# Optimization experiments

Measured on AMD Instinct MI355X. Metric: run time of the kernel, lower is better.

The kernel has to match this reference:

```python
import math
import jax, jax.numpy as jnp
import numpy as np

L, H, C, T_MAX, V = 4, 12, 768, 1024, 50257
D = C // H
EPS = 1e-5


def setup_inputs() -> dict:
    key = jax.random.key(0)
    ks = iter(jax.random.split(key, 32))
    s = 0.02
    inp = {
        "idx": jax.random.randint(next(ks), (2, 1024), 0, V, dtype=jnp.int32),
        "wte": jax.random.normal(next(ks), (V, C), jnp.float32) * s,
        "wpe": jax.random.normal(next(ks), (T_MAX, C), jnp.float32) * s,
        # per-layer stacked params, weights stored [in, out]
        "ln1_w": jnp.ones((L, C), jnp.float32),
        "ln1_b": jnp.zeros((L, C), jnp.float32),
        "qkv_w": jax.random.normal(next(ks), (L, C, 3 * C), jnp.float32) * s,
        "qkv_b": jnp.zeros((L, 3 * C), jnp.float32),
        "proj_w": jax.random.normal(next(ks), (L, C, C), jnp.float32) * (s / math.sqrt(2 * L)),
        "proj_b": jnp.zeros((L, C), jnp.float32),
        "ln2_w": jnp.ones((L, C), jnp.float32),
        "ln2_b": jnp.zeros((L, C), jnp.float32),
        "fc_w": jax.random.normal(next(ks), (L, C, 4 * C), jnp.float32) * s,
        "fc_b": jnp.zeros((L, 4 * C), jnp.float32),
        "fc2_w": jax.random.normal(next(ks), (L, 4 * C, C), jnp.float32) * (s / math.sqrt(2 * L)),
        "fc2_b": jnp.zeros((L, C), jnp.float32),
        "lnf_w": jnp.ones((C,), jnp.float32),
        "lnf_b": jnp.zeros((C,), jnp.float32),
        "head_w": jax.random.normal(next(ks), (C, V), jnp.float32) * s,
    }
    return inp


def _layernorm(x, w, b):
    mu = jnp.mean(x, axis=-1, keepdims=True)
    var = jnp.mean(jnp.square(x - mu), axis=-1, keepdims=True)
    return (x - mu) * jax.lax.rsqrt(var + EPS) * w + b


def _new_gelu(x):
    k = math.sqrt(2.0 / math.pi)
    return 0.5 * x * (1.0 + jnp.tanh(k * (x + 0.044715 * x * x * x)))


def _gpt_forward(idx, wte, wpe, layer_params, lnf_w, lnf_b, head_w):
    B, T = idx.shape
    x = wte[idx] + wpe[:T][None, :, :]  # [B, T, C]
    causal = jnp.tril(jnp.ones((T, T), bool))

    def block(x, p):
        ln1w, ln1b, qkvw, qkvb, pw, pb, ln2w, ln2b, fcw, fcb, fc2w, fc2b = p
        h = _layernorm(x, ln1w, ln1b)
        qkv = h @ qkvw + qkvb  # [B, T, 3C]
        q, k, v = jnp.split(qkv, 3, axis=-1)
        # [B, H, T, D]
        q = q.reshape(B, T, H, D).transpose(0, 2, 1, 3)
        k = k.reshape(B, T, H, D).transpose(0, 2, 1, 3)
        v = v.reshape(B, T, H, D).transpose(0, 2, 1, 3)
        att = jnp.einsum("bhtd,bhsd->bhts", q, k) * (1.0 / math.sqrt(D))
        att = jnp.where(causal, att, -jnp.inf)
        att = jax.nn.softmax(att, axis=-1)
        y = jnp.einsum("bhts,bhsd->bhtd", att, v)
        y = y.transpose(0, 2, 1, 3).reshape(B, T, C)
        x = x + (y @ pw + pb)
        h2 = _layernorm(x, ln2w, ln2b)
        m = _new_gelu(h2 @ fcw + fcb) @ fc2w + fc2b
        return x + m, None

    x, _ = jax.lax.scan(block, x, layer_params)
    x = _layernorm(x, lnf_w, lnf_b)
    logits = x @ head_w  # [B, T, V]
    return logits.reshape(B * T, V)


def reference(idx, wte, wpe, ln1_w, ln1_b, qkv_w, qkv_b, proj_w, proj_b,
              ln2_w, ln2_b, fc_w, fc_b, fc2_w, fc2_b, lnf_w, lnf_b, head_w):
    layer_params = (ln1_w, ln1_b, qkv_w, qkv_b, proj_w, proj_b,
                    ln2_w, ln2_b, fc_w, fc_b, fc2_w, fc2_b)
    return _gpt_forward(idx, wte, wpe, layer_params, lnf_w, lnf_b, head_w)
```

## Files before the change

kernel.cpp:

```cpp
#include <hip/hip_runtime.h>
#include <hip/hip_bf16.h>

typedef __hip_bfloat16 bf16;
typedef __attribute__((ext_vector_type(8))) short bf16x8;
typedef __attribute__((ext_vector_type(4))) float f32x4;
typedef __attribute__((ext_vector_type(4), aligned(4))) float f32x4u;

#define NL 4
#define NH 12
#define C 768
#define T 1024
#define NB 2
#define BTOK 2048
#define V 50257
#define DH 64

__device__ __forceinline__ void gload16(const void* g, void* l) {
  __builtin_amdgcn_global_load_lds(
      (const __attribute__((address_space(1))) void*)g,
      (__attribute__((address_space(3))) void*)l, 16, 0, 0);
}

__device__ __forceinline__ float block_sum(float v, float* red) {
#pragma unroll
  for (int off = 32; off; off >>= 1) v += __shfl_down(v, off);
  int lane = threadIdx.x & 63, wid = threadIdx.x >> 6;
  __syncthreads();
  if (lane == 0) red[wid] = v;
  __syncthreads();
  return red[0] + red[1] + red[2] + red[3];
}

__global__ __launch_bounds__(256) void k_embed(const int* __restrict__ idx,
    const float* __restrict__ wte, const float* __restrict__ wpe,
    float* __restrict__ x) {
  long i = (long)blockIdx.x * 256 + threadIdx.x;
  int bt = (int)(i / C), c = (int)(i % C);
  int t = bt & (T - 1);
  x[i] = wte[(long)idx[bt] * C + c] + wpe[(long)t * C + c];
}

__global__ __launch_bounds__(256) void k_transpose_bf16(const float* __restrict__ W,
    bf16* __restrict__ Wt, int K, int N) {
  __shared__ float tile[32][33];
  long zoff = (long)blockIdx.z * K * N;
  W += zoff;
  Wt += zoff;
  int n0 = blockIdx.x * 32, k0 = blockIdx.y * 32;
  int tx = threadIdx.x, ty = threadIdx.y;
#pragma unroll
  for (int i = 0; i < 4; i++) {
    int k = k0 + ty + i * 8, n = n0 + tx;
    if (k < K && n < N) tile[ty + i * 8][tx] = W[(long)k * N + n];
  }
  __syncthreads();
#pragma unroll
  for (int i = 0; i < 4; i++) {
    int n = n0 + ty + i * 8, k = k0 + tx;
    if (n < N && k < K) Wt[(long)n * K + k] = __float2bfloat16(tile[tx][ty + i * 8]);
  }
}

__global__ __launch_bounds__(256) void k_layernorm(const float* __restrict__ x,
    const float* __restrict__ w, const float* __restrict__ b, bf16* __restrict__ out) {
  __shared__ float red[4];
  long row = blockIdx.x;
  const float* xr = x + row * C;
  int t = threadIdx.x;
  float v0 = xr[t], v1 = xr[t + 256], v2 = xr[t + 512];
  float s = block_sum(v0 + v1 + v2, red);
  float mu = s * (1.0f / C);
  float d0 = v0 - mu, d1 = v1 - mu, d2 = v2 - mu;
  float vs = block_sum(d0 * d0 + d1 * d1 + d2 * d2, red);
  float inv = rsqrtf(vs * (1.0f / C) + 1e-5f);
  bf16* orow = out + row * C;
  orow[t]       = __float2bfloat16(d0 * inv * w[t]       + b[t]);
  orow[t + 256] = __float2bfloat16(d1 * inv * w[t + 256] + b[t + 256]);
  orow[t + 512] = __float2bfloat16(d2 * inv * w[t + 512] + b[t + 512]);
}

__global__ __launch_bounds__(256) void k_attn(const bf16* __restrict__ q,
    const bf16* __restrict__ k, const bf16* __restrict__ vt,
    bf16* __restrict__ yb) {
  __shared__ __align__(16) bf16 Pl[4][16][72];
  int pr = blockIdx.x, bh = blockIdx.y;
  int b = bh / NH, h = bh % NH;
  int tid = threadIdx.x, w = tid >> 6, lane = tid & 63;
  int l15 = lane & 15, hi = lane >> 4;
  const bf16* qbase = q + (long)bh * T * DH;
  const bf16* kbase = k + (long)bh * T * DH;
  const bf16* vbase = vt + (long)bh * DH * T;

  for (int s2 = 0; s2 < 2; s2++) {
    int qt = s2 ? (T / 64 - 1 - pr) : pr;
    int qrow = qt * 64 + w * 16 + l15;
    bf16x8 qf0 = *(const bf16x8*)(qbase + (long)qrow * DH + hi * 8);
    bf16x8 qf1 = *(const bf16x8*)(qbase + (long)qrow * DH + 32 + hi * 8);

    f32x4 accy[4] = {};
    float m_run = -1e30f, l_run = 0.f;

    int nkt = qt + 1;
    for (int kt = 0; kt < nkt; kt++) {
      int kv0 = kt * 64;
      f32x4 accs[4] = {};
#pragma unroll
      for (int kvi = 0; kvi < 4; kvi++) {
        const bf16* kr = kbase + (long)(kv0 + kvi * 16 + l15) * DH + hi * 8;
        bf16x8 kf0 = *(const bf16x8*)kr;
        bf16x8 kf1 = *(const bf16x8*)(kr + 32);
        accs[kvi] = __builtin_amdgcn_mfma_f32_16x16x32_bf16(kf0, qf0, accs[kvi], 0, 0, 0);
        accs[kvi] = __builtin_amdgcn_mfma_f32_16x16x32_bf16(kf1, qf1, accs[kvi], 0, 0, 0);
      }
      bool diag = (kt == qt);
      float p[4][4];
      float tmax = -1e30f;
#pragma unroll
      for (int kvi = 0; kvi < 4; kvi++)
#pragma unroll
        for (int rr = 0; rr < 4; rr++) {
          float s = accs[kvi][rr];
          if (diag && (kvi * 16 + hi * 4 + rr > w * 16 + l15)) s = -1e30f;
          p[kvi][rr] = s;
          tmax = fmaxf(tmax, s);
        }
      tmax = fmaxf(tmax, __shfl_xor(tmax, 16));
      tmax = fmaxf(tmax, __shfl_xor(tmax, 32));
      float m_new = fmaxf(m_run, tmax);
      float scl = __expf(m_run - m_new);
      float psum = 0.f;
#pragma unroll
      for (int kvi = 0; kvi < 4; kvi++)
#pragma unroll
        for (int rr = 0; rr < 4; rr++) {
          float e = __expf(p[kvi][rr] - m_new);
          p[kvi][rr] = e;
          psum += e;
        }
      psum += __shfl_xor(psum, 16);
      psum += __shfl_xor(psum, 32);
      l_run = l_run * scl + psum;
      m_run = m_new;
#pragma unroll
      for (int rr = 0; rr < 4; rr++) {
        float sy = __shfl(scl, hi * 4 + rr);
#pragma unroll
        for (int j = 0; j < 4; j++) accy[j][rr] *= sy;
      }
#pragma unroll
      for (int kvi = 0; kvi < 4; kvi++) {
        union { bf16 hh[2]; unsigned u; } pk0, pk1;
        pk0.hh[0] = __float2bfloat16(p[kvi][0]);
        pk0.hh[1] = __float2bfloat16(p[kvi][1]);
        pk1.hh[0] = __float2bfloat16(p[kvi][2]);
        pk1.hh[1] = __float2bfloat16(p[kvi][3]);
        *(unsigned*)&Pl[w][l15][kvi * 16 + hi * 4]     = pk0.u;
        *(unsigned*)&Pl[w][l15][kvi * 16 + hi * 4 + 2] = pk1.u;
      }
#pragma unroll
      for (int c = 0; c < 2; c++) {
        bf16x8 pf = *(const bf16x8*)&Pl[w][l15][c * 32 + hi * 8];
#pragma unroll
        for (int j = 0; j < 4; j++) {
          const bf16* vr = vbase + (long)(j * 16 + l15) * T + kv0 + c * 32 + hi * 8;
          bf16x8 vf = *(const bf16x8*)vr;
          accy[j] = __builtin_amdgcn_mfma_f32_16x16x32_bf16(pf, vf, accy[j], 0, 0, 0);
        }
      }
    }
    float inv = 1.0f / l_run;
#pragma unroll
    for (int rr = 0; rr < 4; rr++) {
      float li = __shfl(inv, hi * 4 + rr);
      int qg = qt * 64 + w * 16 + hi * 4 + rr;
#pragma unroll
      for (int j = 0; j < 4; j++)
        yb[((long)(b * T + qg)) * C + h * DH + j * 16 + l15] =
            __float2bfloat16(accy[j][rr] * li);
    }
  }
}

__global__ __launch_bounds__(512, 1) void k_head(const bf16* __restrict__ A,
    const bf16* __restrict__ B, float* __restrict__ Cv) {
  __shared__ __align__(16) char lds[131072];
  int hw = blockIdx.y * 8 + blockIdx.x;
  int L = (hw & 7) * 197 + (hw >> 3);
  int mt = L & 7, nt = L >> 3;
  int m0 = mt * 256, n0 = nt * 256;
  int tid = threadIdx.x, lane = tid & 63, wid = tid >> 6;
  int wm = wid >> 2, wn = wid & 3;
  int l15 = lane & 15, hi = lane >> 4, l7 = lane & 7;
  int sg = (lane & 7) ^ (lane >> 3);
  int srA = wid * 8 + (lane >> 3);
  const bf16* Ab = A + (long)(m0 + srA) * 768 + sg * 8;
  const bf16* Bb = B + (long)(n0 + srA) * 768 + sg * 8;
  auto STAGE = [&](int tile, int h) {
    char* dst = lds + (tile & 1) * 65536 + h * 16384 + wid * 1024;
    const bf16* src = (h < 2 ? Ab : Bb) + (long)((h & 1) * 128) * 768 + tile * 64;
    gload16(src, dst);
    gload16(src + 64 * 768, dst + 8192);
  };
  f32x4 acc[8][4] = {};
  STAGE(0, 0); STAGE(0, 1); STAGE(0, 2); STAGE(0, 3); STAGE(1, 0);
  asm volatile("s_waitcnt vmcnt(2)" ::: "memory");
  __builtin_amdgcn_s_barrier();
  int bro = (wn & 1) * 64;
  int g0 = (hi ^ l7) * 16, g1 = ((4 + hi) ^ l7) * 16;
  for (int t = 0; t < 12; t++) {
    char* ha = lds + (t & 1) * 65536 + wm * 16384;
    char* hb = lds + (t & 1) * 65536 + 32768 + (wn >> 1) * 16384;
    bf16x8 af[4], bv[4];
#pragma unroll
    for (int mf = 0; mf < 4; mf++)
      af[mf] = *(const bf16x8*)(ha + (mf * 16 + l15) * 128 + g0);
#pragma unroll
    for (int nf = 0; nf < 4; nf++)
      bv[nf] = *(const bf16x8*)(hb + (bro + nf * 16 + l15) * 128 + g0);
    if (t + 1 < 12) { STAGE(t + 1, 1); STAGE(t + 1, 2); }
    __builtin_amdgcn_s_barrier();
    __builtin_amdgcn_s_setprio(1);
#pragma unroll
    for (int mf = 0; mf < 4; mf++)
#pragma unroll
      for (int nf = 0; nf < 4; nf++)
        acc[mf][nf] = __builtin_amdgcn_mfma_f32_16x16x32_bf16(af[mf], bv[nf], acc[mf][nf], 0, 0, 0);
    __builtin_amdgcn_s_setprio(0);
    __builtin_amdgcn_s_barrier();
#pragma unroll
    for (int mf = 0; mf < 4; mf++)
      af[mf] = *(const bf16x8*)(ha + ((mf + 4) * 16 + l15) * 128 + g0);
    if (t + 1 < 12) STAGE(t + 1, 3);
    __builtin_amdgcn_s_barrier();
    __builtin_amdgcn_s_setprio(1);
#pragma unroll
    for (int mf = 0; mf < 4; mf++)
#pragma unroll
      for (int nf = 0; nf < 4; nf++)
        acc[mf + 4][nf] = __builtin_amdgcn_mfma_f32_16x16x32_bf16(af[mf], bv[nf], acc[mf + 4][nf], 0, 0, 0);
    __builtin_amdgcn_s_setprio(0);
    __builtin_amdgcn_s_barrier();
#pragma unroll
    for (int mf = 0; mf < 4; mf++)
      af[mf] = *(const bf16x8*)(ha + (mf * 16 + l15) * 128 + g1);
#pragma unroll
    for (int nf = 0; nf < 4; nf++)
      bv[nf] = *(const bf16x8*)(hb + (bro + nf * 16 + l15) * 128 + g1);
    __builtin_amdgcn_s_barrier();
    __builtin_amdgcn_s_setprio(1);
#pragma unroll
    for (int mf = 0; mf < 4; mf++)
#pragma unroll
      for (int nf = 0; nf < 4; nf++)
        acc[mf][nf] = __builtin_amdgcn_mfma_f32_16x16x32_bf16(af[mf], bv[nf], acc[mf][nf], 0, 0, 0);
    __builtin_amdgcn_s_setprio(0);
    __builtin_amdgcn_s_barrier();
#pragma unroll
    for (int mf = 0; mf < 4; mf++)
      af[mf] = *(const bf16x8*)(ha + ((mf + 4) * 16 + l15) * 128 + g1);
    if (t + 2 < 12) STAGE(t + 2, 0);
    __builtin_amdgcn_s_barrier();
    __builtin_amdgcn_s_setprio(1);
#pragma unroll
    for (int mf = 0; mf < 4; mf++)
#pragma unroll
      for (int nf = 0; nf < 4; nf++)
        acc[mf + 4][nf] = __builtin_amdgcn_mfma_f32_16x16x32_bf16(af[mf], bv[nf], acc[mf + 4][nf], 0, 0, 0);
    __builtin_amdgcn_s_setprio(0);
    if (t < 11) {
      if (t + 2 < 12) asm volatile("s_waitcnt vmcnt(2)" ::: "memory");
      else            asm volatile("s_waitcnt vmcnt(0)" ::: "memory");
      __builtin_amdgcn_s_barrier();
    }
  }
  __syncthreads();
  float* Cst = (float*)lds;
#pragma unroll
  for (int mf = 0; mf < 8; mf++) {
#pragma unroll
    for (int nf = 0; nf < 4; nf++)
#pragma unroll
      for (int rr = 0; rr < 4; rr++)
        Cst[(wm * 16 + hi * 4 + rr) * 260 + wn * 64 + nf * 16 + l15] = acc[mf][nf][rr];
    __syncthreads();
#pragma unroll
    for (int s = 0; s < 4; s++) {
      int gid = tid + s * 512;
      int r = gid >> 6, g = gid & 63;
      int grow = m0 + (r >> 4) * 128 + mf * 16 + (r & 15);
      int gcol = n0 + g * 4;
      f32x4 vv = *(const f32x4*)&Cst[r * 260 + g * 4];
      float* dst = Cv + (long)grow * V + gcol;
      if (gcol + 3 < V) {
        *(f32x4u*)dst = vv;
      } else {
#pragma unroll
        for (int e = 0; e < 4; e++)
          if (gcol + e < V) dst[e] = vv[e];
      }
    }
    __syncthreads();
  }
}

#define BK 32

template <int EPI, bool SWAPXY>
__global__ __launch_bounds__(256) void k_gemm(const bf16* __restrict__ A,
    const bf16* __restrict__ B, const float* __restrict__ bias,
    void* __restrict__ Cv, int M, int N, int K, int lda, int ldb, int ldc,
    void* __restrict__ Cv2, void* __restrict__ Cv3) {
  __shared__ __align__(16) bf16 As[2][128][BK];
  __shared__ __align__(16) bf16 Bs[2][128][BK];
  int nwg = gridDim.x * gridDim.y;
  int hw = blockIdx.y * gridDim.x + blockIdx.x;
  int logical = (hw & 7) * (nwg >> 3) + (hw >> 3);
  int bx = logical % gridDim.x, by = logical / gridDim.x;
  int m0 = (SWAPXY ? bx : by) * 128;
  int n0 = (SWAPXY ? by : bx) * 128;
  int tid = threadIdx.x;
  int lane = tid & 63, wid = tid >> 6;
  int wr = wid >> 1, wc = wid & 1;
  int l15 = lane & 15, hi = lane >> 4;
  int srow = lane >> 2;
  int scol = (((lane & 3) ^ ((lane >> 3) & 3)) << 3);
  f32x4 acc[4][4] = {};
  const bf16* Ag = A + (long)(m0 + wid * 32 + srow) * lda + scol;
  const bf16* Bg = B + (long)(n0 + wid * 32 + srow) * ldb + scol;
  int NT = K / BK;
  auto STAGE = [&](int t) {
    int k0 = t * BK, b = t & 1;
    gload16(Ag + k0,            &As[b][wid * 32][0]);
    gload16(Ag + k0 + 16 * lda, &As[b][wid * 32 + 16][0]);
    gload16(Bg + k0,            &Bs[b][wid * 32][0]);
    gload16(Bg + k0 + 16 * ldb, &Bs[b][wid * 32 + 16][0]);
  };
  STAGE(0);
  STAGE(1);
  int cA = (hi ^ ((l15 >> 1) & 3)) << 3;
  for (int t = 0; t < NT; t++) {
    int b = t & 1;
    if (t + 1 < NT) asm volatile("s_waitcnt vmcnt(4)" ::: "memory");
    else            asm volatile("s_waitcnt vmcnt(0)" ::: "memory");
    __builtin_amdgcn_s_barrier();
    bf16x8 af[4], bfr[4];
#pragma unroll
    for (int i = 0; i < 4; i++)
      af[i] = *(const bf16x8*)&As[b][wr * 64 + i * 16 + l15][cA];
#pragma unroll
    for (int j = 0; j < 4; j++)
      bfr[j] = *(const bf16x8*)&Bs[b][wc * 64 + j * 16 + l15][cA];
    asm volatile("s_waitcnt lgkmcnt(0)" ::: "memory");
    __builtin_amdgcn_s_barrier();
    if (t + 2 < NT) STAGE(t + 2);
#pragma unroll
    for (int i = 0; i < 4; i++)
#pragma unroll
      for (int j = 0; j < 4; j++)
        acc[i][j] = __builtin_amdgcn_mfma_f32_16x16x32_bf16(af[i], bfr[j], acc[i][j], 0, 0, 0);
  }
#pragma unroll
  for (int j = 0; j < 4; j++) {
    int gn = n0 + wc * 64 + j * 16 + l15;
    if (gn >= N) continue;
    float bv = (bias != nullptr) ? bias[gn] : 0.0f;
#pragma unroll
    for (int i = 0; i < 4; i++) {
#pragma unroll
      for (int rr = 0; rr < 4; rr++) {
        int gm = m0 + wr * 64 + i * 16 + hi * 4 + rr;
        float v = acc[i][j][rr] + bv;
        if constexpr (EPI == 2) {
          float u = 0.7978845608028654f * (v + 0.044715f * v * v * v);
          u = fminf(fmaxf(u, -15.f), 15.f);
          float e2 = __expf(2.f * u);
          float th = (e2 - 1.f) / (e2 + 1.f);
          ((bf16*)Cv)[(long)gm * ldc + gn] = __float2bfloat16(0.5f * v * (1.f + th));
        } else if constexpr (EPI == 5) {
          int gb = gm >> 10, gt = gm & 1023;
          int which = gn / C;
          int r = gn - which * C;
          int h = r >> 6, d = r & 63;
          long bh = (long)(gb * NH + h);
          if (which == 0)
            ((bf16*)Cv)[(bh * T + gt) * DH + d] = __float2bfloat16(v * 0.125f);
          else if (which == 1)
            ((bf16*)Cv2)[(bh * T + gt) * DH + d] = __float2bfloat16(v);
          else
            ((bf16*)Cv3)[(bh * DH + d) * T + gt] = __float2bfloat16(v);
        }
      }
    }
  }
}

#define SBK 64
__global__ __launch_bounds__(256) void k_gemm_s(const bf16* __restrict__ A,
    const bf16* __restrict__ B, const float* __restrict__ bias,
    float* __restrict__ Cx, int M, int N, int K, int lda, int ldb, int ldc) {
  __shared__ __align__(16) bf16 As[2][64][SBK];
  __shared__ __align__(16) bf16 Bs[2][128][SBK];
  int m0 = blockIdx.x * 64, n0 = blockIdx.y * 128;
  int tid = threadIdx.x;
  int lane = tid & 63, w = tid >> 6;
  int l15 = lane & 15, hi = lane >> 4, l7 = lane & 7;
  int srow = lane >> 3;
  int sgr = lane & 7;
  int scol = ((sgr ^ srow) << 3);
  f32x4 acc[4][2] = {};
  const bf16* Ag = A + (long)(m0 + w * 8 + srow) * lda + scol;
  const bf16* Bg = B + (long)(n0 + w * 8 + srow) * ldb + scol;
  int NT = K / SBK;
  auto STAGE = [&](int t) {
    int k0 = t * SBK, b = t & 1;
    gload16(Ag + k0,            &As[b][w * 8][0]);
    gload16(Ag + k0 + 32 * lda, &As[b][w * 8 + 32][0]);
    gload16(Bg + k0,            &Bs[b][w * 8][0]);
    gload16(Bg + k0 + 32 * ldb, &Bs[b][w * 8 + 32][0]);
    gload16(Bg + k0 + 64 * ldb, &Bs[b][w * 8 + 64][0]);
    gload16(Bg + k0 + 96 * ldb, &Bs[b][w * 8 + 96][0]);
  };
  STAGE(0);
  STAGE(1);
  int c0 = (hi ^ l7) << 3, c1 = ((4 + hi) ^ l7) << 3;
  for (int t = 0; t < NT; t++) {
    int b = t & 1;
    if (t + 1 < NT) asm volatile("s_waitcnt vmcnt(6)" ::: "memory");
    else            asm volatile("s_waitcnt vmcnt(0)" ::: "memory");
    __builtin_amdgcn_s_barrier();
    bf16x8 a0[4], a1[4], b0[2], b1[2];
#pragma unroll
    for (int i = 0; i < 4; i++) {
      a0[i] = *(const bf16x8*)&As[b][i * 16 + l15][c0];
      a1[i] = *(const bf16x8*)&As[b][i * 16 + l15][c1];
    }
#pragma unroll
    for (int j = 0; j < 2; j++) {
      b0[j] = *(const bf16x8*)&Bs[b][w * 32 + j * 16 + l15][c0];
      b1[j] = *(const bf16x8*)&Bs[b][w * 32 + j * 16 + l15][c1];
    }
    asm volatile("s_waitcnt lgkmcnt(0)" ::: "memory");
    __builtin_amdgcn_s_barrier();
    if (t + 2 < NT) STAGE(t + 2);
    __builtin_amdgcn_s_setprio(1);
#pragma unroll
    for (int i = 0; i < 4; i++)
#pragma unroll
      for (int j = 0; j < 2; j++) {
        acc[i][j] = __builtin_amdgcn_mfma_f32_16x16x32_bf16(a0[i], b0[j], acc[i][j], 0, 0, 0);
        acc[i][j] = __builtin_amdgcn_mfma_f32_16x16x32_bf16(a1[i], b1[j], acc[i][j], 0, 0, 0);
      }
    __builtin_amdgcn_s_setprio(0);
  }
#pragma unroll
  for (int j = 0; j < 2; j++) {
    int gn = n0 + w * 32 + j * 16 + l15;
    float bv = bias[gn];
#pragma unroll
    for (int i = 0; i < 4; i++)
#pragma unroll
      for (int rr = 0; rr < 4; rr++) {
        int gm = m0 + i * 16 + hi * 4 + rr;
        long off = (long)gm * ldc + gn;
        Cx[off] = acc[i][j][rr] + bv + Cx[off];
      }
  }
}

extern "C" void kernel_launch(void* const* d_in, const int* in_sizes, int n_in,
                              void* d_out, int out_size, void* d_ws, size_t ws_size,
                              hipStream_t stream) {
  const int*   idx    = (const int*)d_in[0];
  const float* wte    = (const float*)d_in[1];
  const float* wpe    = (const float*)d_in[2];
  const float* ln1_w  = (const float*)d_in[3];
  const float* ln1_b  = (const float*)d_in[4];
  const float* qkv_w  = (const float*)d_in[5];
  const float* qkv_b  = (const float*)d_in[6];
  const float* proj_w = (const float*)d_in[7];
  const float* proj_b = (const float*)d_in[8];
  const float* ln2_w  = (const float*)d_in[9];
  const float* ln2_b  = (const float*)d_in[10];
  const float* fc_w   = (const float*)d_in[11];
  const float* fc_b   = (const float*)d_in[12];
  const float* fc2_w  = (const float*)d_in[13];
  const float* fc2_b  = (const float*)d_in[14];
  const float* lnf_w  = (const float*)d_in[15];
  const float* lnf_b  = (const float*)d_in[16];
  const float* head_w = (const float*)d_in[17];
  (void)in_sizes; (void)n_in; (void)out_size; (void)ws_size;

  char* base = (char*)d_ws;
  size_t off = 0;
  auto alloc = [&](size_t bytes) -> void* {
    void* p = base + off;
    off = (off + bytes + 255) & ~(size_t)255;
    return p;
  };
  bf16* wt_qkv  = (bf16*)alloc((size_t)NL * 3 * C * C * 2);
  bf16* wt_proj = (bf16*)alloc((size_t)NL * C * C * 2);
  bf16* wt_fc   = (bf16*)alloc((size_t)NL * 4 * C * C * 2);
  bf16* wt_fc2  = (bf16*)alloc((size_t)NL * 4 * C * C * 2);
  bf16* wt_head = (bf16*)alloc((size_t)V * C * 2);
  float* x      = (float*)alloc((size_t)BTOK * C * 4);
  bf16*  xb     = (bf16*)alloc((size_t)BTOK * C * 2);
  bf16*  qb     = (bf16*)alloc((size_t)NB * NH * T * DH * 2);
  bf16*  kb     = (bf16*)alloc((size_t)NB * NH * T * DH * 2);
  bf16*  vtb    = (bf16*)alloc((size_t)NB * NH * T * DH * 2);
  bf16*  yb     = (bf16*)alloc((size_t)BTOK * C * 2);
  bf16*  mbuf   = (bf16*)alloc((size_t)BTOK * 4 * C * 2);

  dim3 tb(32, 8);
  k_transpose_bf16<<<dim3(72, 24, NL), tb, 0, stream>>>(qkv_w, wt_qkv, C, 3 * C);
  k_transpose_bf16<<<dim3(24, 24, NL), tb, 0, stream>>>(proj_w, wt_proj, C, C);
  k_transpose_bf16<<<dim3(96, 24, NL), tb, 0, stream>>>(fc_w, wt_fc, C, 4 * C);
  k_transpose_bf16<<<dim3(24, 96, NL), tb, 0, stream>>>(fc2_w, wt_fc2, 4 * C, C);
  k_transpose_bf16<<<dim3((V + 31) / 32, 24, 1), tb, 0, stream>>>(head_w, wt_head, C, V);

  k_embed<<<BTOK * C / 256, 256, 0, stream>>>(idx, wte, wpe, x);

  for (int l = 0; l < NL; l++) {
    k_layernorm<<<BTOK, 256, 0, stream>>>(x, ln1_w + l * C, ln1_b + l * C, xb);
    k_gemm<5, true><<<dim3(16, 18), 256, 0, stream>>>(xb, wt_qkv + (long)l * 3 * C * C,
        qkv_b + l * 3 * C, qb, BTOK, 3 * C, C, C, C, 0, kb, vtb);
    k_attn<<<dim3(T / 128, NB * NH), 256, 0, stream>>>(qb, kb, vtb, yb);
    k_gemm_s<<<dim3(32, 6), 256, 0, stream>>>(yb, wt_proj + (long)l * C * C,
        proj_b + l * C, x, BTOK, C, C, C, C, C);
    k_layernorm<<<BTOK, 256, 0, stream>>>(x, ln2_w + l * C, ln2_b + l * C, xb);
    k_gemm<2, true><<<dim3(16, 24), 256, 0, stream>>>(xb, wt_fc + (long)l * 4 * C * C,
        fc_b + l * 4 * C, mbuf, BTOK, 4 * C, C, C, C, 4 * C, nullptr, nullptr);
    k_gemm_s<<<dim3(32, 6), 256, 0, stream>>>(mbuf, wt_fc2 + (long)l * 4 * C * C,
        fc2_b + l * C, x, BTOK, C, 4 * C, 4 * C, 4 * C, C);
  }
  k_layernorm<<<BTOK, 256, 0, stream>>>(x, lnf_w, lnf_b, xb);
  k_head<<<dim3(8, 197), 512, 0, stream>>>(xb, wt_head, (float*)d_out);
}
```

Before: 1.130 ms.

## Unify GEMMs on 64x128 BK64 kernel and batch head epilogue stores

Drops the 128x128 BK=32 GEMM and routes the QKV and FC GEMMs through the 64x128 BK=64 kernel, templated on epilogue type. It also adds XCD-aware block remapping to that kernel. This doubles the workgroup count for those GEMMs to fill more CUs and halves the K-loop iterations. Separately, the LM-head epilogue now stages two m-fragments per LDS round, halving the barriers during the logits write-out. The trade-offs are less operand reuse per block and more LDS staging per round.

```diff
diff --git a/kernel.cpp b/kernel.cpp
--- a/kernel.cpp
+++ b/kernel.cpp
@@ -276,18 +276,23 @@
   __syncthreads();
   float* Cst = (float*)lds;
 #pragma unroll
-  for (int mf = 0; mf < 8; mf++) {
-#pragma unroll
-    for (int nf = 0; nf < 4; nf++)
-#pragma unroll
-      for (int rr = 0; rr < 4; rr++)
-        Cst[(wm * 16 + hi * 4 + rr) * 260 + wn * 64 + nf * 16 + l15] = acc[mf][nf][rr];
+  for (int rnd = 0; rnd < 4; rnd++) {
+#pragma unroll
+    for (int mfl = 0; mfl < 2; mfl++) {
+      int mf = rnd * 2 + mfl;
+#pragma unroll
+      for (int nf = 0; nf < 4; nf++)
+#pragma unroll
+        for (int rr = 0; rr < 4; rr++)
+          Cst[(wm * 32 + mfl * 16 + hi * 4 + rr) * 260 + wn * 64 + nf * 16 + l15] =
+              acc[mf][nf][rr];
+    }
     __syncthreads();
 #pragma unroll
-    for (int s = 0; s < 4; s++) {
+    for (int s = 0; s < 8; s++) {
       int gid = tid + s * 512;
       int r = gid >> 6, g = gid & 63;
-      int grow = m0 + (r >> 4) * 128 + mf * 16 + (r & 15);
+      int grow = m0 + (r >> 5) * 128 + (rnd * 2 + ((r >> 4) & 1)) * 16 + (r & 15);
       int gcol = n0 + g * 4;
       f32x4 vv = *(const f32x4*)&Cst[r * 260 + g * 4];
       float* dst = Cv + (long)grow * V + gcol;
@@ -303,104 +308,19 @@
   }
 }
 
-#define BK 32
-
-template <int EPI, bool SWAPXY>
-__global__ __launch_bounds__(256) void k_gemm(const bf16* __restrict__ A,
+#define SBK 64
+template <int EPI>
+__global__ __launch_bounds__(256) void k_gemm_s(const bf16* __restrict__ A,
     const bf16* __restrict__ B, const float* __restrict__ bias,
     void* __restrict__ Cv, int M, int N, int K, int lda, int ldb, int ldc,
     void* __restrict__ Cv2, void* __restrict__ Cv3) {
-  __shared__ __align__(16) bf16 As[2][128][BK];
-  __shared__ __align__(16) bf16 Bs[2][128][BK];
+  __shared__ __align__(16) bf16 As[2][64][SBK];
+  __shared__ __align__(16) bf16 Bs[2][128][SBK];
   int nwg = gridDim.x * gridDim.y;
   int hw = blockIdx.y * gridDim.x + blockIdx.x;
   int logical = (hw & 7) * (nwg >> 3) + (hw >> 3);
   int bx = logical % gridDim.x, by = logical / gridDim.x;
-  int m0 = (SWAPXY ? bx : by) * 128;
-  int n0 = (SWAPXY ? by : bx) * 128;
-  int tid = threadIdx.x;
-  int lane = tid & 63, wid = tid >> 6;
-  int wr = wid >> 1, wc = wid & 1;
-  int l15 = lane & 15, hi = lane >> 4;
-  int srow = lane >> 2;
-  int scol = (((lane & 3) ^ ((lane >> 3) & 3)) << 3);
-  f32x4 acc[4][4] = {};
-  const bf16* Ag = A + (long)(m0 + wid * 32 + srow) * lda + scol;
-  const bf16* Bg = B + (long)(n0 + wid * 32 + srow) * ldb + scol;
-  int NT = K / BK;
-  auto STAGE = [&](int t) {
-    int k0 = t * BK, b = t & 1;
-    gload16(Ag + k0,            &As[b][wid * 32][0]);
-    gload16(Ag + k0 + 16 * lda, &As[b][wid * 32 + 16][0]);
-    gload16(Bg + k0,            &Bs[b][wid * 32][0]);
-    gload16(Bg + k0 + 16 * ldb, &Bs[b][wid * 32 + 16][0]);
-  };
-  STAGE(0);
-  STAGE(1);
-  int cA = (hi ^ ((l15 >> 1) & 3)) << 3;
-  for (int t = 0; t < NT; t++) {
-    int b = t & 1;
-    if (t + 1 < NT) asm volatile("s_waitcnt vmcnt(4)" ::: "memory");
-    else            asm volatile("s_waitcnt vmcnt(0)" ::: "memory");
-    __builtin_amdgcn_s_barrier();
-    bf16x8 af[4], bfr[4];
-#pragma unroll
-    for (int i = 0; i < 4; i++)
-      af[i] = *(const bf16x8*)&As[b][wr * 64 + i * 16 + l15][cA];
-#pragma unroll
-    for (int j = 0; j < 4; j++)
-      bfr[j] = *(const bf16x8*)&Bs[b][wc * 64 + j * 16 + l15][cA];
-    asm volatile("s_waitcnt lgkmcnt(0)" ::: "memory");
-    __builtin_amdgcn_s_barrier();
-    if (t + 2 < NT) STAGE(t + 2);
-#pragma unroll
-    for (int i = 0; i < 4; i++)
-#pragma unroll
-      for (int j = 0; j < 4; j++)
-        acc[i][j] = __builtin_amdgcn_mfma_f32_16x16x32_bf16(af[i], bfr[j], acc[i][j], 0, 0, 0);
-  }
-#pragma unroll
-  for (int j = 0; j < 4; j++) {
-    int gn = n0 + wc * 64 + j * 16 + l15;
-    if (gn >= N) continue;
-    float bv = (bias != nullptr) ? bias[gn] : 0.0f;
-#pragma unroll
-    for (int i = 0; i < 4; i++) {
-#pragma unroll
-      for (int rr = 0; rr < 4; rr++) {
-        int gm = m0 + wr * 64 + i * 16 + hi * 4 + rr;
-        float v = acc[i][j][rr] + bv;
-        if constexpr (EPI == 2) {
-          float u = 0.7978845608028654f * (v + 0.044715f * v * v * v);
-          u = fminf(fmaxf(u, -15.f), 15.f);
-          float e2 = __expf(2.f * u);
-          float th = (e2 - 1.f) / (e2 + 1.f);
-          ((bf16*)Cv)[(long)gm * ldc + gn] = __float2bfloat16(0.5f * v * (1.f + th));
-        } else if constexpr (EPI == 5) {
-          int gb = gm >> 10, gt = gm & 1023;
-          int which = gn / C;
-          int r = gn - which * C;
-          int h = r >> 6, d = r & 63;
-          long bh = (long)(gb * NH + h);
-          if (which == 0)
-            ((bf16*)Cv)[(bh * T + gt) * DH + d] = __float2bfloat16(v * 0.125f);
-          else if (which == 1)
-            ((bf16*)Cv2)[(bh * T + gt) * DH + d] = __float2bfloat16(v);
-          else
-            ((bf16*)Cv3)[(bh * DH + d) * T + gt] = __float2bfloat16(v);
-        }
-      }
-    }
-  }
-}
-
-#define SBK 64
-__global__ __launch_bounds__(256) void k_gemm_s(const bf16* __restrict__ A,
-    const bf16* __restrict__ B, const float* __restrict__ bias,
-    float* __restrict__ Cx, int M, int N, int K, int lda, int ldb, int ldc) {
-  __shared__ __align__(16) bf16 As[2][64][SBK];
-  __shared__ __align__(16) bf16 Bs[2][128][SBK];
-  int m0 = blockIdx.x * 64, n0 = blockIdx.y * 128;
+  int m0 = bx * 64, n0 = by * 128;
   int tid = threadIdx.x;
   int lane = tid & 63, w = tid >> 6;
   int l15 = lane & 15, hi = lane >> 4, l7 = lane & 7;
@@ -461,8 +381,29 @@
 #pragma unroll
       for (int rr = 0; rr < 4; rr++) {
         int gm = m0 + i * 16 + hi * 4 + rr;
-        long off = (long)gm * ldc + gn;
-        Cx[off] = acc[i][j][rr] + bv + Cx[off];
+        float v = acc[i][j][rr] + bv;
+        if constexpr (EPI == 3) {
+          long off = (long)gm * ldc + gn;
+          ((float*)Cv)[off] = v + ((float*)Cv)[off];
+        } else if constexpr (EPI == 2) {
+          float u = 0.7978845608028654f * (v + 0.044715f * v * v * v);
+          u = fminf(fmaxf(u, -15.f), 15.f);
+          float e2 = __expf(2.f * u);
+          float th = (e2 - 1.f) / (e2 + 1.f);
+          ((bf16*)Cv)[(long)gm * ldc + gn] = __float2bfloat16(0.5f * v * (1.f + th));
+        } else if constexpr (EPI == 5) {
+          int gb = gm >> 10, gt = gm & 1023;
+          int which = gn / C;
+          int r = gn - which * C;
+          int h = r >> 6, d = r & 63;
+          long bh = (long)(gb * NH + h);
+          if (which == 0)
+            ((bf16*)Cv)[(bh * T + gt) * DH + d] = __float2bfloat16(v * 0.125f);
+          else if (which == 1)
+            ((bf16*)Cv2)[(bh * T + gt) * DH + d] = __float2bfloat16(v);
+          else
+            ((bf16*)Cv3)[(bh * DH + d) * T + gt] = __float2bfloat16(v);
+        }
       }
   }
 }
@@ -521,16 +462,16 @@
 
   for (int l = 0; l < NL; l++) {
     k_layernorm<<<BTOK, 256, 0, stream>>>(x, ln1_w + l * C, ln1_b + l * C, xb);
-    k_gemm<5, true><<<dim3(16, 18), 256, 0, stream>>>(xb, wt_qkv + (long)l * 3 * C * C,
+    k_gemm_s<5><<<dim3(32, 18), 256, 0, stream>>>(xb, wt_qkv + (long)l * 3 * C * C,
         qkv_b + l * 3 * C, qb, BTOK, 3 * C, C, C, C, 0, kb, vtb);
     k_attn<<<dim3(T / 128, NB * NH), 256, 0, stream>>>(qb, kb, vtb, yb);
-    k_gemm_s<<<dim3(32, 6), 256, 0, stream>>>(yb, wt_proj + (long)l * C * C,
-        proj_b + l * C, x, BTOK, C, C, C, C, C);
+    k_gemm_s<3><<<dim3(32, 6), 256, 0, stream>>>(yb, wt_proj + (long)l * C * C,
+        proj_b + l * C, x, BTOK, C, C, C, C, C, nullptr, nullptr);
     k_layernorm<<<BTOK, 256, 0, stream>>>(x, ln2_w + l * C, ln2_b + l * C, xb);
-    k_gemm<2, true><<<dim3(16, 24), 256, 0, stream>>>(xb, wt_fc + (long)l * 4 * C * C,
+    k_gemm_s<2><<<dim3(32, 24), 256, 0, stream>>>(xb, wt_fc + (long)l * 4 * C * C,
         fc_b + l * 4 * C, mbuf, BTOK, 4 * C, C, C, C, 4 * C, nullptr, nullptr);
-    k_gemm_s<<<dim3(32, 6), 256, 0, stream>>>(mbuf, wt_fc2 + (long)l * 4 * C * C,
-        fc2_b + l * C, x, BTOK, C, 4 * C, 4 * C, 4 * C, C);
+    k_gemm_s<3><<<dim3(32, 6), 256, 0, stream>>>(mbuf, wt_fc2 + (long)l * 4 * C * C,
+        fc2_b + l * C, x, BTOK, C, 4 * C, 4 * C, 4 * C, C, nullptr, nullptr);
   }
   k_layernorm<<<BTOK, 256, 0, stream>>>(x, lnf_w, lnf_b, xb);
   k_head<<<dim3(8, 197), 512, 0, stream>>>(xb, wt_head, (float*)d_out);
```

Measured after the change: 1.073 ms. 5.1% less time.
